# Performance work log

Hardware: AMD Instinct MI355X
Metric: run time of the kernel (lower is better)

The kernel has to match this reference:

```python
import jax, jax.numpy as jnp
import numpy as np

B, T, D, H, L, V = 2, 1024, 768, 12, 8, 32000
HD = D // H


def setup_inputs() -> dict:
    key = jax.random.key(0)
    ks = jax.random.split(key, 16)
    init = lambda k, shape: jax.random.normal(k, shape, jnp.float32) * 0.02
    return {
        "idx": jax.random.randint(ks[0], (B, T), 0, V),
        "targets": jax.random.randint(ks[1], (B, T), 0, V),
        "tok_emb": init(ks[2], (V, D)),
        "pos_emb": init(ks[3], (T, D)),
        "ln1_w": jnp.ones((L, D)), "ln1_b": jnp.zeros((L, D)),
        "wq": init(ks[4], (L, D, D)),  # per-head D->HD projections stacked columnwise
        "wk": init(ks[5], (L, D, D)),
        "wv": init(ks[6], (L, D, D)),
        "wo": init(ks[7], (L, D, D)), "bo": jnp.zeros((L, D)),
        "ln2_w": jnp.ones((L, D)), "ln2_b": jnp.zeros((L, D)),
        "w1": init(ks[8], (L, D, 4 * D)), "b1": jnp.zeros((L, 4 * D)),
        "w2": init(ks[9], (L, 4 * D, D)), "b2": jnp.zeros((L, D)),
        "lnf_w": jnp.ones((D,)), "lnf_b": jnp.zeros((D,)),
        "lm_w": init(ks[10], (D, V)), "lm_b": jnp.zeros((V,)),
    }


def _ln(x, w, b):
    m = x.mean(-1, keepdims=True)
    v = x.var(-1, keepdims=True)
    return (x - m) * jax.lax.rsqrt(v + 1e-5) * w + b


def _gpt(idx, targets, tok_emb, pos_emb, ln1_w, ln1_b, wq, wk, wv, wo, bo,
         ln2_w, ln2_b, w1, b1, w2, b2, lnf_w, lnf_b, lm_w, lm_b):
    x = tok_emb[idx] + pos_emb[None, :T]          # [B,T,D]
    mask = jnp.tril(jnp.ones((T, T), bool))
    scale = D ** -0.5  # NOTE: original scales by embedding_dim**-0.5 (C), not head_size

    def block(x, p):
        l1w, l1b, Wq, Wk, Wv, Wo, Bo, l2w, l2b, W1, B1, W2, B2 = p
        h = _ln(x, l1w, l1b)
        q = (h @ Wq).reshape(B, T, H, HD)
        k = (h @ Wk).reshape(B, T, H, HD)
        v = (h @ Wv).reshape(B, T, H, HD)
        s = jnp.einsum('bqhd,bkhd->bhqk', q, k) * scale
        s = jnp.where(mask, s, -jnp.inf)
        a = jax.nn.softmax(s, axis=-1)
        o = jnp.einsum('bhqk,bkhd->bqhd', a, v).reshape(B, T, D)
        x = x + o @ Wo + Bo
        h = _ln(x, l2w, l2b)
        x = x + jax.nn.gelu(h @ W1 + B1, approximate=False) @ W2 + B2
        return x, None

    x, _ = jax.lax.scan(block, x, (ln1_w, ln1_b, wq, wk, wv, wo, bo,
                                   ln2_w, ln2_b, w1, b1, w2, b2))
    x = _ln(x, lnf_w, lnf_b)
    logits = (x @ lm_w + lm_b).reshape(B * T, V)
    logp = jax.nn.log_softmax(logits, axis=-1)
    loss = -jnp.take_along_axis(logp, targets.reshape(-1, 1), axis=1).mean()
    return logits, loss


def reference(idx, targets, tok_emb, pos_emb, ln1_w, ln1_b, wq, wk, wv, wo, bo,
              ln2_w, ln2_b, w1, b1, w2, b2, lnf_w, lnf_b, lm_w, lm_b):
    return _gpt(idx, targets, tok_emb, pos_emb, ln1_w, ln1_b, wq, wk, wv, wo, bo,
                ln2_w, ln2_b, w1, b1, w2, b2, lnf_w, lnf_b, lm_w, lm_b)
```

## Files before the change

kernel.cpp:

```cpp
#include <hip/hip_runtime.h>

#define Bz   2
#define Tz   1024
#define Dz   768
#define Hz   12
#define HDz  64
#define Lz   8
#define Vz   32000
#define BTz  (Bz*Tz)
#define DFz  (4*Dz)
#define PLWz 7077888L
#define NPART 500
#define SCALEz 0.036084391824351615f

typedef __attribute__((ext_vector_type(4))) short s16x4;
typedef __attribute__((ext_vector_type(8))) short s16x8;
typedef __attribute__((ext_vector_type(4))) float f32x4;

__device__ __forceinline__ short f2b(float f) {
    union { float f; unsigned u; } v; v.f = f;
    unsigned r = v.u + 0x7fffu + ((v.u >> 16) & 1u);
    return (short)(r >> 16);
}

__device__ __forceinline__ void gload16(const short* g, short* l) {
    __builtin_amdgcn_global_load_lds(
        (const __attribute__((address_space(1))) void*)g,
        (__attribute__((address_space(3))) void*)l, 16, 0, 0);
}

#define MFMA32(a,b,c) __builtin_amdgcn_mfma_f32_16x16x32_bf16(a,b,c,0,0,0)

__global__ __launch_bounds__(256)
void tconv_k(const float* __restrict__ in, short* __restrict__ out,
             int K, int N, int ldin)
{
    __shared__ float tl[32][33];
    const int tx = threadIdx.x & 31, ty = threadIdx.x >> 5;
    const int n0 = blockIdx.x * 32, k0 = blockIdx.y * 32;
    #pragma unroll
    for (int i = 0; i < 4; i++)
        tl[ty + i*8][tx] = in[(long)(k0 + ty + i*8)*ldin + n0 + tx];
    __syncthreads();
    #pragma unroll
    for (int i = 0; i < 4; i++)
        out[(long)(n0 + ty + i*8)*K + k0 + tx] = f2b(tl[tx][ty + i*8]);
}

__global__ __launch_bounds__(256)
void wconv_all(const float* __restrict__ wq, const float* __restrict__ wk,
               const float* __restrict__ wv, const float* __restrict__ wo,
               const float* __restrict__ w1, const float* __restrict__ w2,
               short* __restrict__ wall, int l0)
{
    const int l = l0 + blockIdx.y;
    short* dst = wall + (long)blockIdx.y * PLWz;
    int t = blockIdx.x;
    const float* src; long doff; int K, N, ldin, nx;
    if (t < 2304) {
        int m = t / 576; t -= m * 576;
        src = (m==0 ? wq : m==1 ? wk : m==2 ? wv : wo) + (long)l * 589824;
        doff = (long)m * 589824; K = 768; N = 768; ldin = 768; nx = 24;
    } else if (t < 4608) {
        t -= 2304;
        src = w1 + (long)l * 2359296; doff = 2359296; K = 768; N = 3072; ldin = 3072; nx = 96;
    } else {
        t -= 4608;
        src = w2 + (long)l * 2359296; doff = 4718592; K = 3072; N = 768; ldin = 768; nx = 24;
    }
    const int n0 = (t % nx) * 32, k0 = (t / nx) * 32;
    __shared__ float tl[32][33];
    const int tx = threadIdx.x & 31, ty = threadIdx.x >> 5;
    #pragma unroll
    for (int i = 0; i < 4; i++)
        tl[ty + i*8][tx] = src[(long)(k0 + ty + i*8)*ldin + n0 + tx];
    __syncthreads();
    short* o = dst + doff;
    #pragma unroll
    for (int i = 0; i < 4; i++)
        o[(long)(n0 + ty + i*8)*K + k0 + tx] = f2b(tl[tx][ty + i*8]);
}

template<int BM, int EPI, bool OUTBF, bool SWZ = false, bool LOSSP = false>
__global__ __launch_bounds__(256)
void gemm2(const short* __restrict__ A, const short* __restrict__ Bt,
           const float* __restrict__ bias, const float* __restrict__ resp,
           void* __restrict__ Cv, int K, int ldc, float2* __restrict__ part)
{
    constexpr int BN = 128, BK = 64;
    constexpr int WTM = BM/2;
    constexpr int AM = WTM/16;
    __shared__ short Al[2][BM*BK];
    __shared__ short Bl[2][BN*BK];
    int bx, by;
    if constexpr (SWZ) {
        const int sub = blockIdx.x;
        bx = blockIdx.y*8 + (sub & 7);
        by = sub >> 3;
        if (bx >= Vz/BN) return;
    } else { bx = blockIdx.x; by = blockIdx.y; }
    const int m0 = by*BM, n0 = bx*BN;
    const int tid = threadIdx.x, lane = tid & 63, wid = tid >> 6;
    const int wm = wid >> 1, wn = wid & 1;
    const int r = lane & 15, kg = lane >> 4;
    const int arow = lane >> 3, acol = (lane & 7)*8;

    const short* ga = A  + (long)(m0 + wid*(BM/4) + arow)*K + acol;
    const short* gb = Bt + (long)(n0 + wid*32     + arow)*K + acol;
    const int laoff = (wid*(BM/4))*BK;
    const int lboff = (wid*32)*BK;

    auto stage = [&](int buf, int k0) {
        short* la = &Al[buf][laoff];
        short* lb = &Bl[buf][lboff];
        #pragma unroll
        for (int i = 0; i < BM/32; i++)
            gload16(ga + (long)i*8*K + k0, la + i*8*BK);
        #pragma unroll
        for (int i = 0; i < 4; i++)
            gload16(gb + (long)i*8*K + k0, lb + i*8*BK);
    };

    f32x4 acc[AM][4] = {};
    const int nk = K / BK;

    stage(0, 0);
    __syncthreads();
    int cur = 0;
    for (int t = 0; t < nk; t++) {
        if (t + 1 < nk) stage(cur ^ 1, (t + 1)*BK);
        #pragma unroll
        for (int ks = 0; ks < 2; ks++) {
            s16x8 af[AM], bf[4];
            #pragma unroll
            for (int mI = 0; mI < AM; mI++)
                af[mI] = *(const s16x8*)&Al[cur][(wm*WTM + mI*16 + r)*BK + ks*32 + kg*8];
            #pragma unroll
            for (int nI = 0; nI < 4; nI++)
                bf[nI] = *(const s16x8*)&Bl[cur][(wn*64 + nI*16 + r)*BK + ks*32 + kg*8];
            #pragma unroll
            for (int mI = 0; mI < AM; mI++)
                #pragma unroll
                for (int nI = 0; nI < 4; nI++)
                    acc[mI][nI] = MFMA32(af[mI], bf[nI], acc[mI][nI]);
        }
        __syncthreads();
        cur ^= 1;
    }

    float bnv[4] = {0.f, 0.f, 0.f, 0.f};
    if constexpr (EPI >= 1) {
        #pragma unroll
        for (int nI = 0; nI < 4; nI++) bnv[nI] = bias[n0 + wn*64 + nI*16 + r];
    }

    #pragma unroll
    for (int mI = 0; mI < AM; mI++) {
        #pragma unroll
        for (int nI = 0; nI < 4; nI++) {
            #pragma unroll
            for (int reg = 0; reg < 4; reg++) {
                int row = wm*WTM + mI*16 + kg*4 + reg;
                int col = wn*64 + nI*16 + r;
                long off = (long)(m0+row)*ldc + (n0+col);
                float v = acc[mI][nI][reg] + bnv[nI];
                if constexpr (EPI == 2) v += resp[off];
                if constexpr (EPI == 3) v = 0.5f*v*(1.0f + erff(v*0.70710678118654752f));
                if constexpr (OUTBF) ((short*)Cv)[off] = f2b(v);
                else                 ((float*)Cv)[off] = v;
            }
        }
    }

    if constexpr (LOSSP) {
        #pragma unroll
        for (int mI = 0; mI < AM; mI++) {
            #pragma unroll
            for (int reg = 0; reg < 4; reg++) {
                float mx = -3.4e38f;
                #pragma unroll
                for (int nI = 0; nI < 4; nI++)
                    mx = fmaxf(mx, acc[mI][nI][reg] + bnv[nI]);
                #pragma unroll
                for (int o = 1; o < 16; o <<= 1)
                    mx = fmaxf(mx, __shfl_xor(mx, o));
                float s = 0.f;
                #pragma unroll
                for (int nI = 0; nI < 4; nI++)
                    s += __expf(acc[mI][nI][reg] + bnv[nI] - mx);
                #pragma unroll
                for (int o = 1; o < 16; o <<= 1)
                    s += __shfl_xor(s, o);
                if (r == 0) {
                    int row = m0 + wm*WTM + mI*16 + kg*4 + reg;
                    part[(long)row*NPART + bx*2 + wn] = make_float2(mx, s);
                }
            }
        }
    }
}

__global__ __launch_bounds__(256)
void attn_k(const short* __restrict__ qkv, short* __restrict__ att)
{
    const int w = threadIdx.x >> 6;
    const int lane = threadIdx.x & 63;
    const int r = lane & 15, kg = lane >> 4;
    const int hd0 = blockIdx.y * HDz;
    const long brow = (long)blockIdx.z * Tz;
    const int q0w = blockIdx.x * 64 + w * 16;
    const int qi = q0w + r;

    const short* qp = qkv + (brow + q0w + r) * 2304 + hd0;
    const s16x8 qf0 = *(const s16x8*)(qp + kg*8);
    const s16x8 qf1 = *(const s16x8*)(qp + 32 + kg*8);
    const short* kb = qkv + brow * 2304 + 768 + hd0;
    const short* vb = qkv + brow * 2304 + 1536 + hd0;

    float m = -3.4e38f, l = 0.f;
    f32x4 ot[4] = {};

    const int ntiles = blockIdx.x * 4 + w + 1;
    for (int t = 0; t < ntiles; t++) {
        const int kt = t * 16;
        const short* kp = kb + (long)(kt + r) * 2304;
        s16x8 kf0 = *(const s16x8*)(kp + kg*8);
        s16x8 kf1 = *(const s16x8*)(kp + 32 + kg*8);
        f32x4 z = {};
        f32x4 st = MFMA32(kf0, qf0, z);
        st = MFMA32(kf1, qf1, st);
        float s4[4];
        #pragma unroll
        for (int j = 0; j < 4; j++) {
            int ki = kt + kg*4 + j;
            s4[j] = (ki <= qi) ? st[j]*SCALEz : -1e30f;
        }
        float cm = fmaxf(fmaxf(s4[0], s4[1]), fmaxf(s4[2], s4[3]));
        cm = fmaxf(cm, __shfl_xor(cm, 16));
        cm = fmaxf(cm, __shfl_xor(cm, 32));
        float mn = fmaxf(m, cm);
        float alpha = __expf(m - mn);
        float p0 = __expf(s4[0]-mn), p1 = __expf(s4[1]-mn);
        float p2 = __expf(s4[2]-mn), p3 = __expf(s4[3]-mn);
        l = l*alpha + (p0+p1+p2+p3);
        m = mn;
        s16x8 pb = { f2b(p0), f2b(p1), f2b(p2), f2b(p3), 0, 0, 0, 0 };
        #pragma unroll
        for (int d0 = 0; d0 < 4; d0++) {
            const short* vp = vb + (long)(kt + kg*4)*2304 + d0*16 + r;
            s16x8 va = { vp[0], vp[2304], vp[4608], vp[6912], 0, 0, 0, 0 };
            f32x4 o = ot[d0];
            o[0]*=alpha; o[1]*=alpha; o[2]*=alpha; o[3]*=alpha;
            ot[d0] = MFMA32(va, pb, o);
        }
    }
    l += __shfl_xor(l, 16);
    l += __shfl_xor(l, 32);
    const float inv = 1.f / l;
    short* ap = att + (brow + q0w + r)*Dz + hd0;
    #pragma unroll
    for (int d0 = 0; d0 < 4; d0++) {
        s16x4 pk = { f2b(ot[d0][0]*inv), f2b(ot[d0][1]*inv),
                     f2b(ot[d0][2]*inv), f2b(ot[d0][3]*inv) };
        *(s16x4*)(ap + d0*16 + kg*4) = pk;
    }
}

__global__ void embed_k(const int* __restrict__ idx, const float* __restrict__ tok,
                        const float* __restrict__ pos, float* __restrict__ x)
{
    int qi = blockIdx.x*blockDim.x + threadIdx.x;
    if (qi >= BTz*(Dz/4)) return;
    int row = qi / (Dz/4);
    int c   = (qi % (Dz/4)) * 4;
    int token = idx[row];
    int tpos  = row & (Tz-1);
    float4 a = *reinterpret_cast<const float4*>(tok + (long)token*Dz + c);
    float4 p = *reinterpret_cast<const float4*>(pos + (long)tpos*Dz + c);
    float4 o; o.x=a.x+p.x; o.y=a.y+p.y; o.z=a.z+p.z; o.w=a.w+p.w;
    *reinterpret_cast<float4*>(x + (long)row*Dz + c) = o;
}

__global__ __launch_bounds__(256)
void ln_k(const float* __restrict__ x, const float* __restrict__ w,
          const float* __restrict__ b, short* __restrict__ y)
{
    const int lane = threadIdx.x & 63;
    const int row = blockIdx.x*4 + (threadIdx.x >> 6);
    const float* xr = x + (long)row*Dz;
    float4 v[3];
    #pragma unroll
    for (int j = 0; j < 3; j++) v[j] = *(const float4*)(xr + lane*4 + j*256);
    float s = 0.f, ss = 0.f;
    #pragma unroll
    for (int j = 0; j < 3; j++) {
        s  += v[j].x + v[j].y + v[j].z + v[j].w;
        ss += v[j].x*v[j].x + v[j].y*v[j].y + v[j].z*v[j].z + v[j].w*v[j].w;
    }
    #pragma unroll
    for (int o = 32; o > 0; o >>= 1) {
        s += __shfl_xor(s, o); ss += __shfl_xor(ss, o);
    }
    float mean = s * (1.0f/Dz);
    float var  = ss * (1.0f/Dz) - mean*mean;
    float rs = rsqrtf(var + 1e-5f);
    short* yr = y + (long)row*Dz;
    #pragma unroll
    for (int j = 0; j < 3; j++) {
        float4 wj = *(const float4*)(w + lane*4 + j*256);
        float4 bj = *(const float4*)(b + lane*4 + j*256);
        s16x4 pk = { f2b((v[j].x-mean)*rs*wj.x + bj.x),
                     f2b((v[j].y-mean)*rs*wj.y + bj.y),
                     f2b((v[j].z-mean)*rs*wj.z + bj.z),
                     f2b((v[j].w-mean)*rs*wj.w + bj.w) };
        *(s16x4*)(yr + lane*4 + j*256) = pk;
    }
}

__global__ __launch_bounds__(256)
void lossfin_k(const float* __restrict__ logits, const float2* __restrict__ part,
               const int* __restrict__ tgt, float* __restrict__ row_loss)
{
    const int row = blockIdx.x, t = threadIdx.x;
    float m = -3.4e38f, s = 0.f;
    for (int i = t; i < NPART; i += 256) {
        float2 p = part[(long)row*NPART + i];
        float M = fmaxf(m, p.x);
        s = s*__expf(m - M) + p.y*__expf(p.x - M);
        m = M;
    }
    __shared__ float smm[256], sms[256];
    smm[t] = m; sms[t] = s; __syncthreads();
    for (int k = 128; k > 0; k >>= 1) {
        if (t < k) {
            float M = fmaxf(smm[t], smm[t+k]);
            sms[t] = sms[t]*__expf(smm[t]-M) + sms[t+k]*__expf(smm[t+k]-M);
            smm[t] = M;
        }
        __syncthreads();
    }
    if (t == 0)
        row_loss[row] = smm[0] + logf(sms[0]) - logits[(long)row*Vz + tgt[row]];
}

__global__ __launch_bounds__(256)
void loss_rows_k(const float* __restrict__ logits, const int* __restrict__ tgt,
                 float* __restrict__ row_loss)
{
    int row = blockIdx.x;
    const float* lr = logits + (long)row*Vz;
    const float4* lr4 = (const float4*)lr;
    int t = threadIdx.x;
    __shared__ float sm[256];
    float mx = -3.4e38f;
    for (int c = t; c < Vz/4; c += 256) {
        float4 f = lr4[c];
        mx = fmaxf(mx, fmaxf(fmaxf(f.x, f.y), fmaxf(f.z, f.w)));
    }
    sm[t] = mx; __syncthreads();
    for (int k = 128; k > 0; k >>= 1) { if (t < k) sm[t] = fmaxf(sm[t], sm[t+k]); __syncthreads(); }
    float m = sm[0]; __syncthreads();
    float s = 0.f;
    for (int c = t; c < Vz/4; c += 256) {
        float4 f = lr4[c];
        s += expf(f.x-m) + expf(f.y-m) + expf(f.z-m) + expf(f.w-m);
    }
    sm[t] = s; __syncthreads();
    for (int k = 128; k > 0; k >>= 1) { if (t < k) sm[t] += sm[t+k]; __syncthreads(); }
    if (t == 0) {
        float logZ = m + logf(sm[0]);
        row_loss[row] = logZ - lr[tgt[row]];
    }
}

__global__ void loss_reduce_k(const float* __restrict__ row_loss, float* __restrict__ out)
{
    __shared__ float sm[256];
    int t = threadIdx.x;
    float s = 0.f;
    for (int i = t; i < BTz; i += 256) s += row_loss[i];
    sm[t] = s; __syncthreads();
    for (int k = 128; k > 0; k >>= 1) { if (t < k) sm[t] += sm[t+k]; __syncthreads(); }
    if (t == 0) out[0] = sm[0] * (1.0f/BTz);
}

extern "C" void kernel_launch(void* const* d_in, const int* in_sizes, int n_in,
                              void* d_out, int out_size, void* d_ws, size_t ws_size,
                              hipStream_t stream)
{
    const int*   idx     = (const int*)  d_in[0];
    const int*   tgt     = (const int*)  d_in[1];
    const float* tok_emb = (const float*)d_in[2];
    const float* pos_emb = (const float*)d_in[3];
    const float* ln1_w   = (const float*)d_in[4];
    const float* ln1_b   = (const float*)d_in[5];
    const float* wq      = (const float*)d_in[6];
    const float* wk      = (const float*)d_in[7];
    const float* wv      = (const float*)d_in[8];
    const float* wo      = (const float*)d_in[9];
    const float* bo      = (const float*)d_in[10];
    const float* ln2_w   = (const float*)d_in[11];
    const float* ln2_b   = (const float*)d_in[12];
    const float* w1      = (const float*)d_in[13];
    const float* b1      = (const float*)d_in[14];
    const float* w2      = (const float*)d_in[15];
    const float* b2      = (const float*)d_in[16];
    const float* lnf_w   = (const float*)d_in[17];
    const float* lnf_b   = (const float*)d_in[18];
    const float* lm_w    = (const float*)d_in[19];
    const float* lm_b    = (const float*)d_in[20];

    float* logits = (float*)d_out;
    float* loss   = logits + (long)BTz*Vz;

    char* p = (char*)d_ws;
    float*  x     = (float*)p;  p += (long)BTz*Dz*4;
    float*  rloss = (float*)p;  p += BTz*4;
    float2* part  = (float2*)p; p += (long)BTz*NPART*8;
    short*  h     = (short*)p;  p += (long)BTz*Dz*2;
    short*  qkvb  = (short*)p;  p += (long)BTz*2304*2;
    short*  attb  = (short*)p;  p += (long)BTz*Dz*2;
    short*  midb  = (short*)p;  p += (long)BTz*DFz*2;
    short*  wall  = (short*)p;
    size_t fixed = (size_t)(p - (char*)d_ws);
    const long LMT = (long)Vz*Dz;
    bool upfront = ws_size >= fixed + (size_t)(8*PLWz + LMT)*2;
    short* lmt = wall + (upfront ? 8*PLWz : PLWz);

    embed_k<<<dim3((BTz*(Dz/4) + 255)/256), 256, 0, stream>>>(idx, tok_emb, pos_emb, x);

    if (upfront) {
        wconv_all<<<dim3(6912, 8), 256, 0, stream>>>(wq, wk, wv, wo, w1, w2, wall, 0);
        tconv_k<<<dim3(Vz/32, 24), 256, 0, stream>>>(lm_w, lmt, Dz, Vz, Vz);
    }

    for (int l = 0; l < Lz; l++) {
        short* wl = wall + (upfront ? (long)l*PLWz : 0);
        if (!upfront)
            wconv_all<<<dim3(6912, 1), 256, 0, stream>>>(wq, wk, wv, wo, w1, w2, wall, l);

        ln_k<<<BTz/4, 256, 0, stream>>>(x, ln1_w + l*Dz, ln1_b + l*Dz, h);
        gemm2<128,0,true><<<dim3(18,16), 256, 0, stream>>>(
            h, wl, nullptr, nullptr, qkvb, Dz, 2304, nullptr);
        attn_k<<<dim3(Tz/64, Hz, Bz), 256, 0, stream>>>(qkvb, attb);
        gemm2<64,2,false><<<dim3(6,32), 256, 0, stream>>>(
            attb, wl + 1769472, bo + l*Dz, x, x, Dz, Dz, nullptr);
        ln_k<<<BTz/4, 256, 0, stream>>>(x, ln2_w + l*Dz, ln2_b + l*Dz, h);
        gemm2<128,3,true><<<dim3(24,16), 256, 0, stream>>>(
            h, wl + 2359296, b1 + l*DFz, nullptr, midb, Dz, DFz, nullptr);
        gemm2<64,2,false><<<dim3(6,32), 256, 0, stream>>>(
            midb, wl + 4718592, b2 + l*Dz, x, x, DFz, Dz, nullptr);
    }

    ln_k<<<BTz/4, 256, 0, stream>>>(x, lnf_w, lnf_b, h);
    if (upfront) {
        gemm2<128,1,false,true,true><<<dim3(128, 32), 256, 0, stream>>>(
            h, lmt, lm_b, nullptr, logits, Dz, Vz, part);
        lossfin_k<<<BTz, 256, 0, stream>>>(logits, part, tgt, rloss);
    } else {
        for (int c = 0; c < Vz; c += 8192) {
            int cn = (Vz - c < 8192) ? (Vz - c) : 8192;
            tconv_k<<<dim3(cn/32, 24), 256, 0, stream>>>(lm_w + c, lmt, Dz, cn, Vz);
            gemm2<128,1,false><<<dim3(cn/128, 16), 256, 0, stream>>>(
                h, lmt, lm_b + c, nullptr, logits + c, Dz, Vz, nullptr);
        }
        loss_rows_k<<<BTz, 256, 0, stream>>>(logits, tgt, rloss);
    }
    loss_reduce_k<<<1, 256, 0, stream>>>(rloss, loss);
}
```

Baseline: 1.799 ms.

## Transpose V for contiguous attention loads and add dedicated 256-row LM-head GEMM

Adds a per-layer kernel that transposes the V slice of the QKV buffer into a [B, D, T] layout, so attention loads four consecutive keys as one vector instead of four strided scalar loads. Replaces the swizzled generic GEMM for the LM head with a specialised kernel that uses 256-row tiles and single-buffered LDS, fusing the per-tile softmax partials into its epilogue. The transpose adds an extra kernel launch and more memory traffic in every layer. The LM-head kernel drops double buffering and holds a larger accumulator per thread, which may lower occupancy.

```diff
diff --git a/kernel.cpp b/kernel.cpp
--- a/kernel.cpp
+++ b/kernel.cpp
@@ -81,24 +81,18 @@
         o[(long)(n0 + ty + i*8)*K + k0 + tx] = f2b(tl[tx][ty + i*8]);
 }
 
-template<int BM, int EPI, bool OUTBF, bool SWZ = false, bool LOSSP = false>
+template<int BM, int EPI, bool OUTBF>
 __global__ __launch_bounds__(256)
 void gemm2(const short* __restrict__ A, const short* __restrict__ Bt,
            const float* __restrict__ bias, const float* __restrict__ resp,
-           void* __restrict__ Cv, int K, int ldc, float2* __restrict__ part)
+           void* __restrict__ Cv, int K, int ldc)
 {
     constexpr int BN = 128, BK = 64;
     constexpr int WTM = BM/2;
     constexpr int AM = WTM/16;
     __shared__ short Al[2][BM*BK];
     __shared__ short Bl[2][BN*BK];
-    int bx, by;
-    if constexpr (SWZ) {
-        const int sub = blockIdx.x;
-        bx = blockIdx.y*8 + (sub & 7);
-        by = sub >> 3;
-        if (bx >= Vz/BN) return;
-    } else { bx = blockIdx.x; by = blockIdx.y; }
+    const int bx = blockIdx.x, by = blockIdx.y;
     const int m0 = by*BM, n0 = bx*BN;
     const int tid = threadIdx.x, lane = tid & 63, wid = tid >> 6;
     const int wm = wid >> 1, wn = wid & 1;
@@ -171,37 +165,115 @@
             }
         }
     }
-
-    if constexpr (LOSSP) {
-        #pragma unroll
-        for (int mI = 0; mI < AM; mI++) {
-            #pragma unroll
-            for (int reg = 0; reg < 4; reg++) {
-                float mx = -3.4e38f;
+}
+
+__global__ __launch_bounds__(256, 2)
+void gemm_lm(const short* __restrict__ A, const short* __restrict__ Bt,
+             const float* __restrict__ bias, float* __restrict__ C,
+             float2* __restrict__ part)
+{
+    constexpr int BM = 256, BN = 128, BK = 64;
+    const int b8 = blockIdx.x & 7, rr = blockIdx.x >> 3;
+    const int c  = blockIdx.y * 8 + b8;
+    if (c >= Vz/BN) return;
+    const int m0 = rr * BM, n0 = c * BN;
+    const int K = Dz;
+    __shared__ short Al[BM*BK];
+    __shared__ short Bl[BN*BK];
+    const int tid = threadIdx.x, lane = tid & 63, wid = tid >> 6;
+    const int wm = wid >> 1, wn = wid & 1;
+    const int r = lane & 15, kg = lane >> 4;
+    const int arow = lane >> 3, acol = (lane & 7)*8;
+
+    const short* ga = A  + (long)(m0 + wid*64 + arow)*K + acol;
+    const short* gb = Bt + (long)(n0 + wid*32 + arow)*K + acol;
+    short* la = &Al[(wid*64)*BK];
+    short* lb = &Bl[(wid*32)*BK];
+
+    f32x4 acc[8][4] = {};
+
+    for (int k0 = 0; k0 < K; k0 += BK) {
+        #pragma unroll
+        for (int i = 0; i < 8; i++)
+            gload16(ga + (long)i*8*K + k0, la + i*8*BK);
+        #pragma unroll
+        for (int i = 0; i < 4; i++)
+            gload16(gb + (long)i*8*K + k0, lb + i*8*BK);
+        __syncthreads();
+        #pragma unroll
+        for (int ks = 0; ks < 2; ks++) {
+            s16x8 bf[4];
+            #pragma unroll
+            for (int nI = 0; nI < 4; nI++)
+                bf[nI] = *(const s16x8*)&Bl[(wn*64 + nI*16 + r)*BK + ks*32 + kg*8];
+            #pragma unroll
+            for (int mI = 0; mI < 8; mI++) {
+                s16x8 af = *(const s16x8*)&Al[(wm*128 + mI*16 + r)*BK + ks*32 + kg*8];
                 #pragma unroll
                 for (int nI = 0; nI < 4; nI++)
-                    mx = fmaxf(mx, acc[mI][nI][reg] + bnv[nI]);
-                #pragma unroll
-                for (int o = 1; o < 16; o <<= 1)
-                    mx = fmaxf(mx, __shfl_xor(mx, o));
-                float s = 0.f;
-                #pragma unroll
-                for (int nI = 0; nI < 4; nI++)
-                    s += __expf(acc[mI][nI][reg] + bnv[nI] - mx);
-                #pragma unroll
-                for (int o = 1; o < 16; o <<= 1)
-                    s += __shfl_xor(s, o);
-                if (r == 0) {
-                    int row = m0 + wm*WTM + mI*16 + kg*4 + reg;
-                    part[(long)row*NPART + bx*2 + wn] = make_float2(mx, s);
-                }
+                    acc[mI][nI] = MFMA32(af, bf[nI], acc[mI][nI]);
             }
         }
-    }
-}
-
-__global__ __launch_bounds__(256)
-void attn_k(const short* __restrict__ qkv, short* __restrict__ att)
+        __syncthreads();
+    }
+
+    float bnv[4];
+    #pragma unroll
+    for (int nI = 0; nI < 4; nI++) bnv[nI] = bias[n0 + wn*64 + nI*16 + r];
+
+    #pragma unroll
+    for (int mI = 0; mI < 8; mI++) {
+        #pragma unroll
+        for (int nI = 0; nI < 4; nI++) {
+            #pragma unroll
+            for (int reg = 0; reg < 4; reg++) {
+                int row = wm*128 + mI*16 + kg*4 + reg;
+                int col = wn*64 + nI*16 + r;
+                C[(long)(m0+row)*Vz + (n0+col)] = acc[mI][nI][reg] + bnv[nI];
+            }
+        }
+        #pragma unroll
+        for (int reg = 0; reg < 4; reg++) {
+            float mx = -3.4e38f;
+            #pragma unroll
+            for (int nI = 0; nI < 4; nI++)
+                mx = fmaxf(mx, acc[mI][nI][reg] + bnv[nI]);
+            #pragma unroll
+            for (int o = 1; o < 16; o <<= 1)
+                mx = fmaxf(mx, __shfl_xor(mx, o));
+            float s = 0.f;
+            #pragma unroll
+            for (int nI = 0; nI < 4; nI++)
+                s += __expf(acc[mI][nI][reg] + bnv[nI] - mx);
+            #pragma unroll
+            for (int o = 1; o < 16; o <<= 1)
+                s += __shfl_xor(s, o);
+            if (r == 0) {
+                int row = m0 + wm*128 + mI*16 + kg*4 + reg;
+                part[(long)row*NPART + c*2 + wn] = make_float2(mx, s);
+            }
+        }
+    }
+}
+
+__global__ __launch_bounds__(256)
+void vtrans_k(const short* __restrict__ qkvb, short* __restrict__ vt)
+{
+    __shared__ short tl[64][65];
+    const int t0 = blockIdx.x*64, d0 = blockIdx.y*64, b = blockIdx.z;
+    const int tx = threadIdx.x & 63, ty = threadIdx.x >> 6;
+    #pragma unroll
+    for (int i = 0; i < 16; i++)
+        tl[ty + i*4][tx] = qkvb[((long)b*Tz + t0 + ty + i*4)*2304 + 1536 + d0 + tx];
+    __syncthreads();
+    #pragma unroll
+    for (int i = 0; i < 16; i++)
+        vt[((long)b*Dz + d0 + ty + i*4)*Tz + t0 + tx] = tl[tx][ty + i*4];
+}
+
+__global__ __launch_bounds__(256)
+void attn_k(const short* __restrict__ qkv, const short* __restrict__ vt,
+            short* __restrict__ att)
 {
     const int w = threadIdx.x >> 6;
     const int lane = threadIdx.x & 63;
@@ -215,7 +287,7 @@
     const s16x8 qf0 = *(const s16x8*)(qp + kg*8);
     const s16x8 qf1 = *(const s16x8*)(qp + 32 + kg*8);
     const short* kb = qkv + brow * 2304 + 768 + hd0;
-    const short* vb = qkv + brow * 2304 + 1536 + hd0;
+    const short* vtb = vt + ((long)blockIdx.z*Dz + hd0)*Tz;
 
     float m = -3.4e38f, l = 0.f;
     f32x4 ot[4] = {};
@@ -247,8 +319,8 @@
         s16x8 pb = { f2b(p0), f2b(p1), f2b(p2), f2b(p3), 0, 0, 0, 0 };
         #pragma unroll
         for (int d0 = 0; d0 < 4; d0++) {
-            const short* vp = vb + (long)(kt + kg*4)*2304 + d0*16 + r;
-            s16x8 va = { vp[0], vp[2304], vp[4608], vp[6912], 0, 0, 0, 0 };
+            const s16x4 v4 = *(const s16x4*)(vtb + (long)(d0*16 + r)*Tz + kt + kg*4);
+            s16x8 va = { v4[0], v4[1], v4[2], v4[3], 0, 0, 0, 0 };
             f32x4 o = ot[d0];
             o[0]*=alpha; o[1]*=alpha; o[2]*=alpha; o[3]*=alpha;
             ot[d0] = MFMA32(va, pb, o);
@@ -419,6 +491,7 @@
     float2* part  = (float2*)p; p += (long)BTz*NPART*8;
     short*  h     = (short*)p;  p += (long)BTz*Dz*2;
     short*  qkvb  = (short*)p;  p += (long)BTz*2304*2;
+    short*  vt    = (short*)p;  p += (long)Bz*Dz*Tz*2;
     short*  attb  = (short*)p;  p += (long)BTz*Dz*2;
     short*  midb  = (short*)p;  p += (long)BTz*DFz*2;
     short*  wall  = (short*)p;
@@ -441,28 +514,28 @@
 
         ln_k<<<BTz/4, 256, 0, stream>>>(x, ln1_w + l*Dz, ln1_b + l*Dz, h);
         gemm2<128,0,true><<<dim3(18,16), 256, 0, stream>>>(
-            h, wl, nullptr, nullptr, qkvb, Dz, 2304, nullptr);
-        attn_k<<<dim3(Tz/64, Hz, Bz), 256, 0, stream>>>(qkvb, attb);
+            h, wl, nullptr, nullptr, qkvb, Dz, 2304);
+        vtrans_k<<<dim3(Tz/64, Dz/64, Bz), 256, 0, stream>>>(qkvb, vt);
+        attn_k<<<dim3(Tz/64, Hz, Bz), 256, 0, stream>>>(qkvb, vt, attb);
         gemm2<64,2,false><<<dim3(6,32), 256, 0, stream>>>(
-            attb, wl + 1769472, bo + l*Dz, x, x, Dz, Dz, nullptr);
+            attb, wl + 1769472, bo + l*Dz, x, x, Dz, Dz);
         ln_k<<<BTz/4, 256, 0, stream>>>(x, ln2_w + l*Dz, ln2_b + l*Dz, h);
         gemm2<128,3,true><<<dim3(24,16), 256, 0, stream>>>(
-            h, wl + 2359296, b1 + l*DFz, nullptr, midb, Dz, DFz, nullptr);
+            h, wl + 2359296, b1 + l*DFz, nullptr, midb, Dz, DFz);
         gemm2<64,2,false><<<dim3(6,32), 256, 0, stream>>>(
-            midb, wl + 4718592, b2 + l*Dz, x, x, DFz, Dz, nullptr);
+            midb, wl + 4718592, b2 + l*Dz, x, x, DFz, Dz);
     }
 
     ln_k<<<BTz/4, 256, 0, stream>>>(x, lnf_w, lnf_b, h);
     if (upfront) {
-        gemm2<128,1,false,true,true><<<dim3(128, 32), 256, 0, stream>>>(
-            h, lmt, lm_b, nullptr, logits, Dz, Vz, part);
+        gemm_lm<<<dim3(64, 32), 256, 0, stream>>>(h, lmt, lm_b, logits, part);
         lossfin_k<<<BTz, 256, 0, stream>>>(logits, part, tgt, rloss);
     } else {
         for (int c = 0; c < Vz; c += 8192) {
             int cn = (Vz - c < 8192) ? (Vz - c) : 8192;
             tconv_k<<<dim3(cn/32, 24), 256, 0, stream>>>(lm_w + c, lmt, Dz, cn, Vz);
             gemm2<128,1,false><<<dim3(cn/128, 16), 256, 0, stream>>>(
-                h, lmt, lm_b + c, nullptr, logits + c, Dz, Vz, nullptr);
+                h, lmt, lm_b + c, nullptr, logits + c, Dz, Vz);
         }
         loss_rows_k<<<BTz, 256, 0, stream>>>(logits, tgt, rloss);
     }
```

After: 2.068 ms. +15.0%, slower.
